# Optimization experiments

Hardware: AMD Instinct MI355X
Metric: run time of the kernel (lower is better)

Reference implementation:

```python
import jax, jax.numpy as jnp
import numpy as np

IN_FEATURES = 3072
OUT_FEATURES = 12288
BLOCK = 32  # GGML Q8_0 block size


def setup_inputs() -> dict:
    key = jax.random.key(0)
    k_x, k_q, k_s, k_b = jax.random.split(key, 4)
    n_blocks = IN_FEATURES // BLOCK
    x = jax.random.normal(k_x, (4096, IN_FEATURES), dtype=jnp.float32)
    # int8-valued quants stored per Q8_0 block (kept as int32 carrier dtype)
    w_q = jax.random.randint(k_q, (OUT_FEATURES, n_blocks, BLOCK), -127, 128, dtype=jnp.int32)
    # one fp scale per 32-element block (small magnitude, like real d-values)
    scales = jax.random.uniform(k_s, (OUT_FEATURES, n_blocks, 1), dtype=jnp.float32) * 0.01
    bias = jax.random.normal(k_b, (OUT_FEATURES,), dtype=jnp.float32) * 0.02
    return {"x": x, "w_q": w_q, "scales": scales, "bias": bias}


def reference(x, w_q, scales, bias):
    # Block dequantization (GGML Q8_0: w = scale * int8_quant per 32-block),
    # materializing the full fp weight exactly as DequantingLinear.forward does,
    # then a standard F.linear: y = x @ W^T + b.
    out_f, n_blocks, block = w_q.shape
    W = (w_q.astype(x.dtype) * scales.astype(x.dtype)).reshape(out_f, n_blocks * block)
    return jnp.einsum("ti,oi->to", x, W) + bias.astype(x.dtype)
```

## Files before the change

kernel.cpp:

```cpp
#include <hip/hip_runtime.h>
#include <hip/hip_bf16.h>

typedef __bf16 bf16_t;
typedef __bf16 bf16x8 __attribute__((ext_vector_type(8)));
typedef float  f32x4  __attribute__((ext_vector_type(4)));
typedef int    i32x4  __attribute__((ext_vector_type(4)));
typedef signed char i8x16 __attribute__((ext_vector_type(16)));

#define M_DIM 4096
#define N_DIM 12288
#define K_DIM 3072
#define NBLK  96

#define BM 256
#define BN 256
#define BKB 128
#define THREADS 512
#define NT (K_DIM / BKB)

#define W8_OFF  ((size_t)0)
#define X8_OFF  ((size_t)N_DIM * K_DIM)
#define RO_OFF  (X8_OFF + (size_t)M_DIM * K_DIM)
#define ROI_OFF (RO_OFF + (size_t)N_DIM * 4)
#define SX_OFF  (ROI_OFF + (size_t)N_DIM * 4)
#define SXI_OFF (SX_OFF + (size_t)M_DIM * 4)
#define WS_NEED (SXI_OFF + (size_t)M_DIM * 4)

#define WQB (N_DIM * K_DIM / 16 / 256)
#define XQB (M_DIM * K_DIM / 16 / 256)

#define BAR()   asm volatile("s_barrier" ::: "memory")
#define SBAR()  __builtin_amdgcn_sched_barrier(0)

__device__ __forceinline__ void gload_lds16(const void* g, void* l) {
    __builtin_amdgcn_global_load_lds(
        (const __attribute__((address_space(1))) unsigned int*)g,
        (__attribute__((address_space(3))) unsigned int*)l, 16, 0, 0);
}

__global__ __launch_bounds__(256) void romax_kernel(
    const float* __restrict__ scales, float* __restrict__ Ro,
    float* __restrict__ RoInv)
{
    int o = blockIdx.x * 256 + threadIdx.x;
    const float* p = scales + (size_t)o * NBLK;
    float mx = 1e-20f;
#pragma unroll
    for (int i = 0; i < 24; ++i) {
        f32x4 v = *(const f32x4*)(p + i * 4);
        mx = fmaxf(mx, fmaxf(fmaxf(v[0], v[1]), fmaxf(v[2], v[3])));
    }
    Ro[o] = mx;
    RoInv[o] = 1.f / mx;
}

__global__ __launch_bounds__(256) void xmax_kernel(
    const float* __restrict__ x, float* __restrict__ Sx,
    float* __restrict__ SxInv)
{
    int row = blockIdx.x;
    const float* p = x + (size_t)row * K_DIM;
    float mx = 1e-20f;
#pragma unroll
    for (int i = 0; i < 3; ++i) {
        f32x4 v = *(const f32x4*)(p + i * 1024 + threadIdx.x * 4);
        mx = fmaxf(mx, fmaxf(fmaxf(fabsf(v[0]), fabsf(v[1])),
                             fmaxf(fabsf(v[2]), fabsf(v[3]))));
    }
#pragma unroll
    for (int off = 32; off; off >>= 1) mx = fmaxf(mx, __shfl_xor(mx, off));
    __shared__ float red[4];
    if ((threadIdx.x & 63) == 0) red[threadIdx.x >> 6] = mx;
    __syncthreads();
    if (threadIdx.x == 0) {
        mx = fmaxf(fmaxf(red[0], red[1]), fmaxf(red[2], red[3]));
        Sx[row] = mx / 127.f;
        SxInv[row] = 127.f / mx;
    }
}

__global__ __launch_bounds__(256) void quant_kernel(
    const int* __restrict__ wq, const float* __restrict__ scales,
    const float* __restrict__ RoInv, const float* __restrict__ x,
    const float* __restrict__ SxInv,
    signed char* __restrict__ W8, signed char* __restrict__ X8)
{
    unsigned b = blockIdx.x;
    if (b < WQB) {
        unsigned c = b * 256u + threadIdx.x;
        unsigned o = c / 192u;
        unsigned j = c - o * 192u;
        float f = scales[o * NBLK + (j >> 1)] * RoInv[o];
        const int* gq = wq + (size_t)c * 16;
        i8x16 v;
#pragma unroll
        for (int i = 0; i < 4; ++i) {
            i32x4 q = *(const i32x4*)(gq + i * 4);
            v[i * 4 + 0] = (signed char)__float2int_rn((float)q[0] * f);
            v[i * 4 + 1] = (signed char)__float2int_rn((float)q[1] * f);
            v[i * 4 + 2] = (signed char)__float2int_rn((float)q[2] * f);
            v[i * 4 + 3] = (signed char)__float2int_rn((float)q[3] * f);
        }
        *(i8x16*)&W8[(size_t)c * 16] = v;
    } else {
        unsigned c = (b - WQB) * 256u + threadIdx.x;
        unsigned row = c / 192u;
        float f = SxInv[row];
        const float* gp = x + (size_t)c * 16;
        i8x16 v;
#pragma unroll
        for (int i = 0; i < 4; ++i) {
            f32x4 g = *(const f32x4*)(gp + i * 4);
            v[i * 4 + 0] = (signed char)__float2int_rn(g[0] * f);
            v[i * 4 + 1] = (signed char)__float2int_rn(g[1] * f);
            v[i * 4 + 2] = (signed char)__float2int_rn(g[2] * f);
            v[i * 4 + 3] = (signed char)__float2int_rn(g[3] * f);
        }
        *(i8x16*)&X8[(size_t)c * 16] = v;
    }
}

__global__ __launch_bounds__(THREADS, 2) void gemm_i8_kernel(
    const signed char* __restrict__ A8, const signed char* __restrict__ B8,
    const float* __restrict__ Ro, const float* __restrict__ Sx,
    const float* __restrict__ bias, float* __restrict__ out)
{
    __shared__ __align__(16) signed char sA8[2][BM * BKB];
    __shared__ __align__(16) signed char sB8[2][BN * BKB];

    const int tid  = threadIdx.x;
    const int bm   = blockIdx.x / (N_DIM / BN);
    const int bn   = blockIdx.x % (N_DIM / BN);
    const int row0 = bm * BM;
    const int col0 = bn * BN;

    const int lane = tid & 63;
    const int wid  = tid >> 6;
    const int wr   = (wid >> 2) * 128;
    const int wc   = (wid & 3) * 64;
    const int fr   = lane & 15;
    const int kq   = lane >> 4;

    const int rws = tid >> 3;
    const int c8s = (tid & 7) ^ (rws & 7);
    const signed char* srcA = A8 + (size_t)(row0 + rws) * K_DIM + c8s * 16;
    const signed char* srcB = B8 + (size_t)(col0 + rws) * K_DIM + c8s * 16;
    const int ldsU = (tid & ~63) * 16;

    auto stA = [&](int d, int uh, int tt) {
        const signed char* s = srcA + (size_t)tt * BKB + (size_t)uh * 128 * K_DIM;
        gload_lds16(s,                        &sA8[d][uh * 16384 + ldsU]);
        gload_lds16(s + (size_t)64 * K_DIM,   &sA8[d][uh * 16384 + 8192 + ldsU]);
    };
    auto stB = [&](int d, int uh, int tt) {
        const signed char* s = srcB + (size_t)tt * BKB + (size_t)uh * 128 * K_DIM;
        gload_lds16(s,                        &sB8[d][uh * 16384 + ldsU]);
        gload_lds16(s + (size_t)64 * K_DIM,   &sB8[d][uh * 16384 + 8192 + ldsU]);
    };

    i32x4 acc[8][4];
#pragma unroll
    for (int m = 0; m < 8; ++m)
#pragma unroll
        for (int n = 0; n < 4; ++n) acc[m][n] = (i32x4)0;

    auto rdA = [&](const signed char* pA, int rbase, i32x4 (&dst)[4][2]) {
#pragma unroll
        for (int m = 0; m < 4; ++m) {
            int row = rbase + m * 16 + fr;
#pragma unroll
            for (int ks = 0; ks < 2; ++ks) {
                int kc = ks * 4 + kq;
                dst[m][ks] = *(const i32x4*)(pA + row * BKB + ((kc ^ (row & 7)) << 4));
            }
        }
    };
    auto rdB = [&](const signed char* pB, int rbase, i32x4 (&dst)[2][2]) {
#pragma unroll
        for (int n = 0; n < 2; ++n) {
            int row = rbase + n * 16 + fr;
#pragma unroll
            for (int ks = 0; ks < 2; ++ks) {
                int kc = ks * 4 + kq;
                dst[n][ks] = *(const i32x4*)(pB + row * BKB + ((kc ^ (row & 7)) << 4));
            }
        }
    };
    auto mm = [&](i32x4 (&a)[4][2], i32x4 (&b)[2][2], int mo, int no) {
        __builtin_amdgcn_s_setprio(1);
#pragma unroll
        for (int m = 0; m < 4; ++m)
#pragma unroll
            for (int n = 0; n < 2; ++n)
#pragma unroll
                for (int ks = 0; ks < 2; ++ks)
                    acc[mo + m][no + n] = __builtin_amdgcn_mfma_i32_16x16x64_i8(
                        a[m][ks], b[n][ks], acc[mo + m][no + n], 0, 0, 0);
        __builtin_amdgcn_s_setprio(0);
    };

    i32x4 af0a[4][2], af1a[4][2], bg0a[2][2], bg1a[2][2];
    i32x4 af0b[4][2], af1b[4][2], bg0b[2][2], bg1b[2][2];

    stA(0, 0, 0); stA(0, 1, 0); stB(0, 0, 0); stB(0, 1, 0);
    stA(1, 0, 1); stA(1, 1, 1);
    asm volatile("s_waitcnt vmcnt(4)" ::: "memory");
    BAR();
    rdA(&sA8[0][0], wr, af0a); rdB(&sB8[0][0], wc, bg0a);

    auto ktile = [&](int cur, int t,
                     i32x4 (&AF0)[4][2], i32x4 (&AF1)[4][2],
                     i32x4 (&BG0)[2][2], i32x4 (&BG1)[2][2],
                     i32x4 (&AF0n)[4][2], i32x4 (&BG0n)[2][2]) {
        const signed char* pA  = &sA8[cur][0];
        const signed char* pB  = &sB8[cur][0];
        const signed char* pAn = &sA8[cur ^ 1][0];
        const signed char* pBn = &sB8[cur ^ 1][0];
        int t1 = t + 1; if (t1 >= NT) t1 -= NT;
        int t2 = t + 2; if (t2 >= NT) t2 -= NT;

        rdA(pA, wr + 64, AF1);
        stB(cur ^ 1, 0, t1);
        SBAR();
        mm(AF0, BG0, 0, 0);

        rdB(pB, wc + 32, BG1);
        stB(cur ^ 1, 1, t1);
        SBAR();
        mm(AF1, BG0, 4, 0);
        BAR();

        stA(cur, 0, t2);
        stA(cur, 1, t2);
        SBAR();
        mm(AF1, BG1, 4, 2);
        SBAR();
        asm volatile("s_waitcnt vmcnt(4)" ::: "memory");
        BAR();

        rdA(pAn, wr, AF0n); rdB(pBn, wc, BG0n);
        SBAR();
        mm(AF0, BG1, 0, 2);
    };

    for (int it = 0; it < NT / 2; ++it) {
        ktile(0, it * 2,     af0a, af1a, bg0a, bg1a, af0b, bg0b);
        ktile(1, it * 2 + 1, af0b, af1b, bg0b, bg1b, af0a, bg0a);
    }

    const int crow = (lane >> 4) << 2;
    const int ccol = lane & 15;
    float ro[4], bb[4];
#pragma unroll
    for (int n = 0; n < 4; ++n) {
        int col = col0 + wc + n * 16 + ccol;
        ro[n] = Ro[col];
        bb[n] = bias[col];
    }
#pragma unroll
    for (int m = 0; m < 8; ++m) {
#pragma unroll
        for (int j = 0; j < 4; ++j) {
            int row = row0 + wr + m * 16 + crow + j;
            float sx = Sx[row];
            size_t base = (size_t)row * N_DIM + col0 + wc + ccol;
#pragma unroll
            for (int n = 0; n < 4; ++n)
                out[base + n * 16] = (float)acc[m][n][j] * ro[n] * sx + bb[n];
        }
    }
}

#define FBM 128
#define FBN 128
#define FBK 64
#define FTHREADS 256
__global__ __launch_bounds__(FTHREADS) void dq_gemm_fused_kernel(
    const float* __restrict__ x, const int* __restrict__ wq,
    const float* __restrict__ scales, const float* __restrict__ bias,
    float* __restrict__ out)
{
    __shared__ bf16_t fA[FBM * FBK];
    __shared__ bf16_t fB[FBN * FBK];

    const int tid  = threadIdx.x;
    const int bm   = blockIdx.x / (N_DIM / FBN);
    const int bn   = blockIdx.x % (N_DIM / FBN);
    const int row0 = bm * FBM;
    const int col0 = bn * FBN;
    const int lane = tid & 63;
    const int wid  = tid >> 6;
    const int wr   = (wid >> 1) * 64;
    const int wc   = (wid & 1) * 64;
    const int fr   = lane & 15;
    const int fk   = (lane >> 4) << 3;

    f32x4 acc[4][4];
#pragma unroll
    for (int m = 0; m < 4; ++m)
#pragma unroll
        for (int n = 0; n < 4; ++n) acc[m][n] = (f32x4)0.f;

    for (int kt = 0; kt < K_DIM / FBK; ++kt) {
        const int kb = kt * FBK;
#pragma unroll
        for (int c = 0; c < 4; ++c) {
            int i  = c * FTHREADS + tid;
            int r  = i >> 3;
            int k0 = (i & 7) << 3;
            const float* gp = x + (size_t)(row0 + r) * K_DIM + kb + k0;
            f32x4 f0 = *(const f32x4*)gp;
            f32x4 f1 = *(const f32x4*)(gp + 4);
            bf16x8 v;
            v[0] = (bf16_t)f0[0]; v[1] = (bf16_t)f0[1];
            v[2] = (bf16_t)f0[2]; v[3] = (bf16_t)f0[3];
            v[4] = (bf16_t)f1[0]; v[5] = (bf16_t)f1[1];
            v[6] = (bf16_t)f1[2]; v[7] = (bf16_t)f1[3];
            *(bf16x8*)&fA[r * FBK + (k0 ^ ((r & 7) << 3))] = v;
        }
#pragma unroll
        for (int c = 0; c < 4; ++c) {
            int i  = c * FTHREADS + tid;
            int r  = i >> 3;
            int k0 = (i & 7) << 3;
            int o  = col0 + r;
            const int* gq = wq + (size_t)o * K_DIM + kb + k0;
            i32x4 q0 = *(const i32x4*)gq;
            i32x4 q1 = *(const i32x4*)(gq + 4);
            float s = scales[o * NBLK + ((kb + k0) >> 5)];
            bf16x8 v;
            v[0] = (bf16_t)((float)q0[0] * s); v[1] = (bf16_t)((float)q0[1] * s);
            v[2] = (bf16_t)((float)q0[2] * s); v[3] = (bf16_t)((float)q0[3] * s);
            v[4] = (bf16_t)((float)q1[0] * s); v[5] = (bf16_t)((float)q1[1] * s);
            v[6] = (bf16_t)((float)q1[2] * s); v[7] = (bf16_t)((float)q1[3] * s);
            *(bf16x8*)&fB[r * FBK + (k0 ^ ((r & 7) << 3))] = v;
        }
        __syncthreads();
#pragma unroll
        for (int ks = 0; ks < 2; ++ks) {
            bf16x8 af[4], bg[4];
#pragma unroll
            for (int m = 0; m < 4; ++m) {
                int r = wr + m * 16 + fr;
                af[m] = *(const bf16x8*)&fA[r * FBK + ((ks * 32 + fk) ^ ((r & 7) << 3))];
            }
#pragma unroll
            for (int n = 0; n < 4; ++n) {
                int r = wc + n * 16 + fr;
                bg[n] = *(const bf16x8*)&fB[r * FBK + ((ks * 32 + fk) ^ ((r & 7) << 3))];
            }
#pragma unroll
            for (int m = 0; m < 4; ++m)
#pragma unroll
                for (int n = 0; n < 4; ++n)
                    acc[m][n] = __builtin_amdgcn_mfma_f32_16x16x32_bf16(
                        af[m], bg[n], acc[m][n], 0, 0, 0);
        }
        __syncthreads();
    }

    const int crow = (lane >> 4) << 2;
    const int ccol = lane & 15;
#pragma unroll
    for (int m = 0; m < 4; ++m) {
#pragma unroll
        for (int n = 0; n < 4; ++n) {
            int col = col0 + wc + n * 16 + ccol;
            float b = bias[col];
#pragma unroll
            for (int j = 0; j < 4; ++j) {
                int row = row0 + wr + m * 16 + crow + j;
                out[(size_t)row * N_DIM + col] = acc[m][n][j] + b;
            }
        }
    }
}

extern "C" void kernel_launch(void* const* d_in, const int* in_sizes, int n_in,
                              void* d_out, int out_size, void* d_ws, size_t ws_size,
                              hipStream_t stream) {
    const float* x      = (const float*)d_in[0];
    const int*   wq     = (const int*)d_in[1];
    const float* scales = (const float*)d_in[2];
    const float* bias   = (const float*)d_in[3];
    float*       out    = (float*)d_out;

    if (ws_size >= WS_NEED) {
        signed char* W8    = (signed char*)d_ws + W8_OFF;
        signed char* X8    = (signed char*)d_ws + X8_OFF;
        float*       Ro    = (float*)((char*)d_ws + RO_OFF);
        float*       RoInv = (float*)((char*)d_ws + ROI_OFF);
        float*       Sx    = (float*)((char*)d_ws + SX_OFF);
        float*       SxInv = (float*)((char*)d_ws + SXI_OFF);

        romax_kernel<<<dim3(N_DIM / 256), dim3(256), 0, stream>>>(scales, Ro, RoInv);
        xmax_kernel<<<dim3(M_DIM), dim3(256), 0, stream>>>(x, Sx, SxInv);
        quant_kernel<<<dim3(WQB + XQB), dim3(256), 0, stream>>>(
            wq, scales, RoInv, x, SxInv, W8, X8);
        gemm_i8_kernel<<<dim3((M_DIM / BM) * (N_DIM / BN)), dim3(THREADS), 0, stream>>>(
            X8, W8, Ro, Sx, bias, out);
    } else {
        dq_gemm_fused_kernel<<<dim3((M_DIM / FBM) * (N_DIM / FBN)), dim3(FTHREADS), 0, stream>>>(
            x, wq, scales, bias, out);
    }
}
```

Measured before the change: 209.5 us.

## Fuse x row-max with quantization and load GEMM B fragments directly from global

The separate x max-reduction and x quantization passes are merged into one per-row kernel that keeps the loaded values in registers, so x is read once instead of twice. Weight quantization gets its own kernel. In the int8 GEMM, the B operand is no longer staged through shared memory: each wave loads its B MFMA fragments straight from global memory into registers, one tile ahead, which halves the shared-memory footprint and drops the B LDS writes and reads. The cost is more uncoalesced global loads for B, heavier register pressure, and global latency sitting on the MFMA critical path. The vmcnt waits were not retuned, and they now also count the direct B loads.

```diff
diff --git a/kernel.cpp b/kernel.cpp
--- a/kernel.cpp
+++ b/kernel.cpp
@@ -23,11 +23,9 @@
 #define RO_OFF  (X8_OFF + (size_t)M_DIM * K_DIM)
 #define ROI_OFF (RO_OFF + (size_t)N_DIM * 4)
 #define SX_OFF  (ROI_OFF + (size_t)N_DIM * 4)
-#define SXI_OFF (SX_OFF + (size_t)M_DIM * 4)
-#define WS_NEED (SXI_OFF + (size_t)M_DIM * 4)
+#define WS_NEED (SX_OFF + (size_t)M_DIM * 4)
 
 #define WQB (N_DIM * K_DIM / 16 / 256)
-#define XQB (M_DIM * K_DIM / 16 / 256)
 
 #define BAR()   asm volatile("s_barrier" ::: "memory")
 #define SBAR()  __builtin_amdgcn_sched_barrier(0)
@@ -54,79 +52,67 @@
     RoInv[o] = 1.f / mx;
 }
 
-__global__ __launch_bounds__(256) void xmax_kernel(
+__global__ __launch_bounds__(256) void xprep_kernel(
     const float* __restrict__ x, float* __restrict__ Sx,
-    float* __restrict__ SxInv)
-{
-    int row = blockIdx.x;
+    signed char* __restrict__ X8)
+{
+    const int row = blockIdx.x;
+    const int tid = threadIdx.x;
     const float* p = x + (size_t)row * K_DIM;
+    f32x4 v[3];
     float mx = 1e-20f;
 #pragma unroll
     for (int i = 0; i < 3; ++i) {
-        f32x4 v = *(const f32x4*)(p + i * 1024 + threadIdx.x * 4);
-        mx = fmaxf(mx, fmaxf(fmaxf(fabsf(v[0]), fabsf(v[1])),
-                             fmaxf(fabsf(v[2]), fabsf(v[3]))));
+        v[i] = *(const f32x4*)(p + i * 1024 + tid * 4);
+        mx = fmaxf(mx, fmaxf(fmaxf(fabsf(v[i][0]), fabsf(v[i][1])),
+                             fmaxf(fabsf(v[i][2]), fabsf(v[i][3]))));
     }
 #pragma unroll
     for (int off = 32; off; off >>= 1) mx = fmaxf(mx, __shfl_xor(mx, off));
     __shared__ float red[4];
-    if ((threadIdx.x & 63) == 0) red[threadIdx.x >> 6] = mx;
+    if ((tid & 63) == 0) red[tid >> 6] = mx;
     __syncthreads();
-    if (threadIdx.x == 0) {
-        mx = fmaxf(fmaxf(red[0], red[1]), fmaxf(red[2], red[3]));
-        Sx[row] = mx / 127.f;
-        SxInv[row] = 127.f / mx;
-    }
-}
-
-__global__ __launch_bounds__(256) void quant_kernel(
+    mx = fmaxf(fmaxf(red[0], red[1]), fmaxf(red[2], red[3]));
+    if (tid == 0) Sx[row] = mx / 127.f;
+    const float f = 127.f / mx;
+    signed char* xo = X8 + (size_t)row * K_DIM;
+#pragma unroll
+    for (int i = 0; i < 3; ++i) {
+        unsigned b0 = (unsigned)__float2int_rn(v[i][0] * f) & 0xffu;
+        unsigned b1 = (unsigned)__float2int_rn(v[i][1] * f) & 0xffu;
+        unsigned b2 = (unsigned)__float2int_rn(v[i][2] * f) & 0xffu;
+        unsigned b3 = (unsigned)__float2int_rn(v[i][3] * f) & 0xffu;
+        *(unsigned*)&xo[i * 1024 + tid * 4] = b0 | (b1 << 8) | (b2 << 16) | (b3 << 24);
+    }
+}
+
+__global__ __launch_bounds__(256) void wquant_kernel(
     const int* __restrict__ wq, const float* __restrict__ scales,
-    const float* __restrict__ RoInv, const float* __restrict__ x,
-    const float* __restrict__ SxInv,
-    signed char* __restrict__ W8, signed char* __restrict__ X8)
-{
-    unsigned b = blockIdx.x;
-    if (b < WQB) {
-        unsigned c = b * 256u + threadIdx.x;
-        unsigned o = c / 192u;
-        unsigned j = c - o * 192u;
-        float f = scales[o * NBLK + (j >> 1)] * RoInv[o];
-        const int* gq = wq + (size_t)c * 16;
-        i8x16 v;
-#pragma unroll
-        for (int i = 0; i < 4; ++i) {
-            i32x4 q = *(const i32x4*)(gq + i * 4);
-            v[i * 4 + 0] = (signed char)__float2int_rn((float)q[0] * f);
-            v[i * 4 + 1] = (signed char)__float2int_rn((float)q[1] * f);
-            v[i * 4 + 2] = (signed char)__float2int_rn((float)q[2] * f);
-            v[i * 4 + 3] = (signed char)__float2int_rn((float)q[3] * f);
-        }
-        *(i8x16*)&W8[(size_t)c * 16] = v;
-    } else {
-        unsigned c = (b - WQB) * 256u + threadIdx.x;
-        unsigned row = c / 192u;
-        float f = SxInv[row];
-        const float* gp = x + (size_t)c * 16;
-        i8x16 v;
-#pragma unroll
-        for (int i = 0; i < 4; ++i) {
-            f32x4 g = *(const f32x4*)(gp + i * 4);
-            v[i * 4 + 0] = (signed char)__float2int_rn(g[0] * f);
-            v[i * 4 + 1] = (signed char)__float2int_rn(g[1] * f);
-            v[i * 4 + 2] = (signed char)__float2int_rn(g[2] * f);
-            v[i * 4 + 3] = (signed char)__float2int_rn(g[3] * f);
-        }
-        *(i8x16*)&X8[(size_t)c * 16] = v;
-    }
-}
-
-__global__ __launch_bounds__(THREADS, 2) void gemm_i8_kernel(
+    const float* __restrict__ RoInv, signed char* __restrict__ W8)
+{
+    unsigned c = blockIdx.x * 256u + threadIdx.x;
+    unsigned o = c / 192u;
+    unsigned j = c - o * 192u;
+    float f = scales[o * NBLK + (j >> 1)] * RoInv[o];
+    const int* gq = wq + (size_t)c * 16;
+    i8x16 v;
+#pragma unroll
+    for (int i = 0; i < 4; ++i) {
+        i32x4 q = *(const i32x4*)(gq + i * 4);
+        v[i * 4 + 0] = (signed char)__float2int_rn((float)q[0] * f);
+        v[i * 4 + 1] = (signed char)__float2int_rn((float)q[1] * f);
+        v[i * 4 + 2] = (signed char)__float2int_rn((float)q[2] * f);
+        v[i * 4 + 3] = (signed char)__float2int_rn((float)q[3] * f);
+    }
+    *(i8x16*)&W8[(size_t)c * 16] = v;
+}
+
+__global__ __launch_bounds__(THREADS, 2) void gemm_i8d_kernel(
     const signed char* __restrict__ A8, const signed char* __restrict__ B8,
     const float* __restrict__ Ro, const float* __restrict__ Sx,
     const float* __restrict__ bias, float* __restrict__ out)
 {
     __shared__ __align__(16) signed char sA8[2][BM * BKB];
-    __shared__ __align__(16) signed char sB8[2][BN * BKB];
 
     const int tid  = threadIdx.x;
     const int bm   = blockIdx.x / (N_DIM / BN);
@@ -144,7 +130,6 @@
     const int rws = tid >> 3;
     const int c8s = (tid & 7) ^ (rws & 7);
     const signed char* srcA = A8 + (size_t)(row0 + rws) * K_DIM + c8s * 16;
-    const signed char* srcB = B8 + (size_t)(col0 + rws) * K_DIM + c8s * 16;
     const int ldsU = (tid & ~63) * 16;
 
     auto stA = [&](int d, int uh, int tt) {
@@ -152,10 +137,15 @@
         gload_lds16(s,                        &sA8[d][uh * 16384 + ldsU]);
         gload_lds16(s + (size_t)64 * K_DIM,   &sA8[d][uh * 16384 + 8192 + ldsU]);
     };
-    auto stB = [&](int d, int uh, int tt) {
-        const signed char* s = srcB + (size_t)tt * BKB + (size_t)uh * 128 * K_DIM;
-        gload_lds16(s,                        &sB8[d][uh * 16384 + ldsU]);
-        gload_lds16(s + (size_t)64 * K_DIM,   &sB8[d][uh * 16384 + 8192 + ldsU]);
+
+    const signed char* gB = B8 + (size_t)(col0 + wc + fr) * K_DIM + kq * 16;
+    auto loadB = [&](i32x4 (&BG)[4][2], int tt) {
+#pragma unroll
+        for (int n = 0; n < 4; ++n)
+#pragma unroll
+            for (int ks = 0; ks < 2; ++ks)
+                BG[n][ks] = *(const i32x4*)(gB + (size_t)(n * 16) * K_DIM
+                                              + (size_t)tt * BKB + ks * 64);
     };
 
     i32x4 acc[8][4];
@@ -175,18 +165,7 @@
             }
         }
     };
-    auto rdB = [&](const signed char* pB, int rbase, i32x4 (&dst)[2][2]) {
-#pragma unroll
-        for (int n = 0; n < 2; ++n) {
-            int row = rbase + n * 16 + fr;
-#pragma unroll
-            for (int ks = 0; ks < 2; ++ks) {
-                int kc = ks * 4 + kq;
-                dst[n][ks] = *(const i32x4*)(pB + row * BKB + ((kc ^ (row & 7)) << 4));
-            }
-        }
-    };
-    auto mm = [&](i32x4 (&a)[4][2], i32x4 (&b)[2][2], int mo, int no) {
+    auto mm = [&](i32x4 (&a)[4][2], i32x4 (&BG)[4][2], int nb, int mo, int no) {
         __builtin_amdgcn_s_setprio(1);
 #pragma unroll
         for (int m = 0; m < 4; ++m)
@@ -195,57 +174,55 @@
 #pragma unroll
                 for (int ks = 0; ks < 2; ++ks)
                     acc[mo + m][no + n] = __builtin_amdgcn_mfma_i32_16x16x64_i8(
-                        a[m][ks], b[n][ks], acc[mo + m][no + n], 0, 0, 0);
+                        a[m][ks], BG[nb + n][ks], acc[mo + m][no + n], 0, 0, 0);
         __builtin_amdgcn_s_setprio(0);
     };
 
-    i32x4 af0a[4][2], af1a[4][2], bg0a[2][2], bg1a[2][2];
-    i32x4 af0b[4][2], af1b[4][2], bg0b[2][2], bg1b[2][2];
-
-    stA(0, 0, 0); stA(0, 1, 0); stB(0, 0, 0); stB(0, 1, 0);
+    i32x4 af0a[4][2], af0b[4][2];
+    i32x4 BGa[4][2],  BGb[4][2];
+
+    stA(0, 0, 0); stA(0, 1, 0);
+    loadB(BGa, 0);
     stA(1, 0, 1); stA(1, 1, 1);
     asm volatile("s_waitcnt vmcnt(4)" ::: "memory");
     BAR();
-    rdA(&sA8[0][0], wr, af0a); rdB(&sB8[0][0], wc, bg0a);
+    rdA(&sA8[0][0], wr, af0a);
 
     auto ktile = [&](int cur, int t,
-                     i32x4 (&AF0)[4][2], i32x4 (&AF1)[4][2],
-                     i32x4 (&BG0)[2][2], i32x4 (&BG1)[2][2],
-                     i32x4 (&AF0n)[4][2], i32x4 (&BG0n)[2][2]) {
+                     i32x4 (&AF0)[4][2], i32x4 (&BG)[4][2],
+                     i32x4 (&AF0n)[4][2], i32x4 (&BGn)[4][2]) {
         const signed char* pA  = &sA8[cur][0];
-        const signed char* pB  = &sB8[cur][0];
         const signed char* pAn = &sA8[cur ^ 1][0];
-        const signed char* pBn = &sB8[cur ^ 1][0];
         int t1 = t + 1; if (t1 >= NT) t1 -= NT;
         int t2 = t + 2; if (t2 >= NT) t2 -= NT;
 
+        i32x4 AF1[4][2];
+
         rdA(pA, wr + 64, AF1);
-        stB(cur ^ 1, 0, t1);
-        SBAR();
-        mm(AF0, BG0, 0, 0);
-
-        rdB(pB, wc + 32, BG1);
-        stB(cur ^ 1, 1, t1);
-        SBAR();
-        mm(AF1, BG0, 4, 0);
+        loadB(BGn, t1);
+        SBAR();
+        mm(AF0, BG, 0, 0, 0);
+
+        SBAR();
+        mm(AF1, BG, 0, 4, 0);
         BAR();
 
         stA(cur, 0, t2);
         stA(cur, 1, t2);
         SBAR();
-        mm(AF1, BG1, 4, 2);
+        mm(AF1, BG, 2, 4, 2);
         SBAR();
         asm volatile("s_waitcnt vmcnt(4)" ::: "memory");
         BAR();
 
-        rdA(pAn, wr, AF0n); rdB(pBn, wc, BG0n);
-        SBAR();
-        mm(AF0, BG1, 0, 2);
+        rdA(pAn, wr, AF0n);
+        SBAR();
+        mm(AF0, BG, 2, 0, 2);
     };
 
     for (int it = 0; it < NT / 2; ++it) {
-        ktile(0, it * 2,     af0a, af1a, bg0a, bg1a, af0b, bg0b);
-        ktile(1, it * 2 + 1, af0b, af1b, bg0b, bg1b, af0a, bg0a);
+        ktile(0, it * 2,     af0a, BGa, af0b, BGb);
+        ktile(1, it * 2 + 1, af0b, BGb, af0a, BGa);
     }
 
     const int crow = (lane >> 4) << 2;
@@ -391,13 +368,11 @@
         float*       Ro    = (float*)((char*)d_ws + RO_OFF);
         float*       RoInv = (float*)((char*)d_ws + ROI_OFF);
         float*       Sx    = (float*)((char*)d_ws + SX_OFF);
-        float*       SxInv = (float*)((char*)d_ws + SXI_OFF);
 
         romax_kernel<<<dim3(N_DIM / 256), dim3(256), 0, stream>>>(scales, Ro, RoInv);
-        xmax_kernel<<<dim3(M_DIM), dim3(256), 0, stream>>>(x, Sx, SxInv);
-        quant_kernel<<<dim3(WQB + XQB), dim3(256), 0, stream>>>(
-            wq, scales, RoInv, x, SxInv, W8, X8);
-        gemm_i8_kernel<<<dim3((M_DIM / BM) * (N_DIM / BN)), dim3(THREADS), 0, stream>>>(
+        xprep_kernel<<<dim3(M_DIM), dim3(256), 0, stream>>>(x, Sx, X8);
+        wquant_kernel<<<dim3(WQB), dim3(256), 0, stream>>>(wq, scales, RoInv, W8);
+        gemm_i8d_kernel<<<dim3((M_DIM / BM) * (N_DIM / BN)), dim3(THREADS), 0, stream>>>(
             X8, W8, Ro, Sx, bias, out);
     } else {
         dq_gemm_fused_kernel<<<dim3((M_DIM / FBM) * (N_DIM / FBN)), dim3(FTHREADS), 0, stream>>>(
```

Result: slower. 398.4 us (+90.1%).
